# Kernel tuning notes

Hardware: AMD Instinct MI355X
Metric: run time of the kernel (lower is better)

## Reference

```python
import jax, jax.numpy as jnp
import numpy as np

EMBED_DIM = 1024
NUM_HEADS = 16
HEAD_DIM = EMBED_DIM // NUM_HEADS


def setup_inputs() -> dict:
    key = jax.random.key(0)
    ks = jax.random.split(key, 7)
    B, S, D = 2, 2048, EMBED_DIM
    scale = 1.0 / np.sqrt(D)
    return {
        "query": jax.random.normal(ks[0], (B, S, D), dtype=jnp.float32),
        "key": jax.random.normal(ks[1], (B, S, D), dtype=jnp.float32),
        "value": jax.random.normal(ks[2], (B, S, D), dtype=jnp.float32),
        "W_qkv": jax.random.normal(ks[3], (D, 3 * D), dtype=jnp.float32) * scale,
        "b_qkv": jnp.zeros((3 * D,), dtype=jnp.float32),
        "W_out": jax.random.normal(ks[4], (D, D), dtype=jnp.float32) * scale,
        "b_out": jnp.zeros((D,), dtype=jnp.float32),
    }


def reference(query, key, value, W_qkv, b_qkv, W_out, b_out):
    # NOTE: the original torch forward ignores `key` and `value` — q,k,v all
    # come from qkv_proj(query). We keep them as args for signature fidelity.
    B, S, D = query.shape
    H, hd = NUM_HEADS, HEAD_DIM
    scale = hd ** -0.5

    qkv = query @ W_qkv + b_qkv                      # [B, S, 3D]
    qkv = qkv.reshape(B, S, 3, H, hd)
    q = jnp.transpose(qkv[:, :, 0], (0, 2, 1, 3))    # [B, H, S, hd]
    k = jnp.transpose(qkv[:, :, 1], (0, 2, 1, 3))
    v = jnp.transpose(qkv[:, :, 2], (0, 2, 1, 3))

    scores = jnp.einsum("bhsd,bhtd->bhst", q, k) * scale  # [B, H, S, S]
    attn = jax.nn.softmax(scores, axis=-1)
    out = jnp.einsum("bhst,bhtd->bhsd", attn, v)           # [B, H, S, hd]
    out = jnp.transpose(out, (0, 2, 1, 3)).reshape(B, S, D)
    return out @ W_out + b_out
```

## Files before the change

### kernel.cpp

```cpp
#include <hip/hip_runtime.h>
#include <stdint.h>

#define DEV static __device__ __forceinline__

typedef __attribute__((ext_vector_type(4))) float f32x4;
typedef __attribute__((ext_vector_type(8))) short bf16x8;
typedef bf16x8 __attribute__((may_alias)) bf16x8_a;
typedef __attribute__((ext_vector_type(2))) unsigned int u32x2;
typedef u32x2 __attribute__((may_alias)) u32x2_a;

DEV unsigned short f2bf(float f) {
  union { float f; unsigned int u; } v; v.f = f;
  return (unsigned short)((v.u + 0x7FFFu + ((v.u >> 16) & 1u)) >> 16);
}

DEV float bf2f(unsigned short s) {
  union { unsigned int u; float f; } v; v.u = ((unsigned int)s) << 16;
  return v.f;
}

DEV float fast_exp2(float x) {
  float r;
  asm("v_exp_f32 %0, %1" : "=v"(r) : "v"(x));
  return r;
}

DEV unsigned int pktrunc(float lo, float hi) {
  union { float f; unsigned int u; } a, b; a.f = lo; b.f = hi;
  return __builtin_amdgcn_perm(b.u, a.u, 0x07060302u);
}

DEV void gload_lds16(const void* g, void* l) {
  __builtin_amdgcn_global_load_lds(
      (const __attribute__((address_space(1))) unsigned int*)g,
      (__attribute__((address_space(3))) unsigned int*)l, 16, 0, 0);
}

__global__ void cast_bf16_k(const float4* __restrict__ in, ushort4* __restrict__ out, int n4) {
  int i = blockIdx.x * 256 + threadIdx.x;
  if (i >= n4) return;
  float4 f = in[i];
  ushort4 o; o.x = f2bf(f.x); o.y = f2bf(f.y); o.z = f2bf(f.z); o.w = f2bf(f.w);
  out[i] = o;
}

__global__ __launch_bounds__(256) void transpose_bf16_k(const float* __restrict__ in,
                                                        unsigned short* __restrict__ out,
                                                        int R, int C) {
  __shared__ float tile[32][33];
  const int t = threadIdx.x;
  const int r = t >> 3, c4 = (t & 7) << 2;
  const int tr = blockIdx.y << 5, tc = blockIdx.x << 5;
  const float4 v = *(const float4*)(in + (size_t)(tr + r) * C + tc + c4);
  tile[r][c4] = v.x; tile[r][c4 + 1] = v.y; tile[r][c4 + 2] = v.z; tile[r][c4 + 3] = v.w;
  __syncthreads();
  ushort4 o;
  o.x = f2bf(tile[c4][r]); o.y = f2bf(tile[c4 + 1][r]);
  o.z = f2bf(tile[c4 + 2][r]); o.w = f2bf(tile[c4 + 3][r]);
  *(ushort4*)(out + (size_t)(tc + r) * R + tr + c4) = o;
}

template <int EPI, int BN>
__global__ __launch_bounds__(256) void gemm_bt(const unsigned short* __restrict__ A,
                                               const unsigned short* __restrict__ BT,
                                               const float* __restrict__ bias,
                                               float* __restrict__ Cout,
                                               unsigned short* __restrict__ q_buf,
                                               unsigned short* __restrict__ k_buf,
                                               unsigned short* __restrict__ vT_buf,
                                               int M, int N, int K) {
  constexpr int MI = (BN == 128) ? 4 : 2;
  constexpr int MW = MI * 16;
  __shared__ unsigned short As[2][128 * 32];
  __shared__ unsigned short Bs[2][BN * 32];
  const int t = threadIdx.x, w = t >> 6, l = t & 63;
  const int wm = (BN == 128) ? (w >> 1) : w;
  const int wn = (BN == 128) ? (w & 1) : 0;
  const int lg = l >> 4, ln = l & 15;

  const int xcd = blockIdx.x & 7, jb = blockIdx.x >> 3;
  const int m0 = (xcd * 4 + (jb & 3)) * 128;
  const int n0 = (jb >> 2) * BN;

  const int srow = w * 16 + (l >> 2);
  const int schunk = (l & 3) ^ ((l >> 3) & 3);
  const int dchunk = l & 3;

  f32x4 acc[MI][4] = {};

#define STAGE_G(buf, k0)                                                                              \
  do {                                                                                                \
    gload_lds16(A + (size_t)(m0 + srow) * K + (k0) + schunk * 8, &As[buf][srow * 32 + dchunk * 8]);   \
    gload_lds16(A + (size_t)(m0 + srow + 64) * K + (k0) + schunk * 8,                                 \
                &As[buf][(srow + 64) * 32 + dchunk * 8]);                                             \
    gload_lds16(BT + (size_t)(n0 + srow) * K + (k0) + schunk * 8, &Bs[buf][srow * 32 + dchunk * 8]);  \
    if (BN == 128)                                                                                    \
      gload_lds16(BT + (size_t)(n0 + srow + 64) * K + (k0) + schunk * 8,                              \
                  &Bs[buf][(srow + 64) * 32 + dchunk * 8]);                                           \
  } while (0)

  STAGE_G(0, 0);
  __syncthreads();

  const int rsw = (ln >> 1) & 3;
  const int rchunk = (lg ^ rsw) << 3;
  const int nit = K >> 5;
  for (int it = 0; it < nit; ++it) {
    const int buf = it & 1;
    if (it + 1 < nit) STAGE_G(buf ^ 1, (it + 1) * 32);

    bf16x8 af[MI], bfr[4];
#pragma unroll
    for (int mi = 0; mi < MI; ++mi)
      af[mi] = *(const bf16x8_a*)&As[buf][(wm * MW + mi * 16 + ln) * 32 + rchunk];
#pragma unroll
    for (int ni = 0; ni < 4; ++ni)
      bfr[ni] = *(const bf16x8_a*)&Bs[buf][(wn * 64 + ni * 16 + ln) * 32 + rchunk];
#pragma unroll
    for (int mi = 0; mi < MI; ++mi)
#pragma unroll
      for (int ni = 0; ni < 4; ++ni)
        acc[mi][ni] = __builtin_amdgcn_mfma_f32_16x16x32_bf16(af[mi], bfr[ni], acc[mi][ni], 0, 0, 0);

    __syncthreads();
  }
#undef STAGE_G

#pragma unroll
  for (int ni = 0; ni < 4; ++ni) {
    const int c = n0 + wn * 64 + ni * 16 + ln;
    const float bv = bias[c];
    if (EPI == 1) {
      const int which = c >> 10;
      const int h = (c >> 6) & 15;
      const int d = c & 63;
#pragma unroll
      for (int mi = 0; mi < MI; ++mi) {
        const int mrow = m0 + wm * MW + mi * 16 + lg * 4;
        const int b = mrow >> 11, s = mrow & 2047;
        const size_t bh = (size_t)(b * 16 + h);
        f32x4 v = acc[mi][ni];
        if (which == 0) {
          const float QSCALE = 0.125f * 1.44269504088896340736f;
          unsigned short* dst = q_buf + (bh * 2048 + s) * 64 + d;
#pragma unroll
          for (int r = 0; r < 4; ++r) dst[(size_t)r * 64] = f2bf((v[r] + bv) * QSCALE);
        } else if (which == 1) {
          unsigned short* dst = k_buf + (bh * 2048 + s) * 64 + d;
#pragma unroll
          for (int r = 0; r < 4; ++r) dst[(size_t)r * 64] = f2bf(v[r] + bv);
        } else {
          unsigned short* dst = vT_buf + (bh * 64 + d) * 2048 + s;
          ushort4 o4;
          o4.x = f2bf(v[0] + bv); o4.y = f2bf(v[1] + bv); o4.z = f2bf(v[2] + bv); o4.w = f2bf(v[3] + bv);
          *(ushort4*)dst = o4;
        }
      }
    } else {
#pragma unroll
      for (int mi = 0; mi < MI; ++mi) {
        const int mrow = m0 + wm * MW + mi * 16 + lg * 4;
        f32x4 v = acc[mi][ni];
#pragma unroll
        for (int r = 0; r < 4; ++r) Cout[(size_t)(mrow + r) * N + c] = v[r] + bv;
      }
    }
  }
}

template <int SPLIT>
__global__ __launch_bounds__(256, 3) void attn_k(const unsigned short* __restrict__ Qb,
                                                 const unsigned short* __restrict__ Kb,
                                                 const unsigned short* __restrict__ Vt,
                                                 unsigned short* __restrict__ AO,
                                                 unsigned short* __restrict__ Opart,
                                                 float* __restrict__ lpart) {
  constexpr int NT = 32 / SPLIT;
  const float SHIFT = -15.9943754f;
  const float CINV  = 0.99610895f;
  __shared__ unsigned short Ks[2][64 * 64];
  __shared__ unsigned short Vs[2][64 * 64];
  __shared__ unsigned short Ps[4][32 * 64];

  const int t = threadIdx.x, w = t >> 6, l = t & 63;
  const int lg = l >> 4, ln = l & 15;
  const int xcd = blockIdx.x & 7, idx = blockIdx.x >> 3;
  const int bh = xcd * 4 + (idx & 3);
  const int qt = (SPLIT == 2) ? ((idx >> 2) & 15) : (idx >> 2);
  const int half = (SPLIT == 2) ? (idx >> 6) : 0;
  const int b = bh >> 4, h = bh & 15;
  const unsigned short* Q = Qb + (size_t)bh * 2048 * 64;
  const unsigned short* K = Kb + (size_t)bh * 2048 * 64 + (size_t)half * NT * 64 * 64;
  const unsigned short* V = Vt + (size_t)bh * 64 * 2048 + half * NT * 64;
  const int qbase = qt * 128 + w * 32;

  const int srow = t >> 3;
  const int scol = ((t & 7) ^ (srow & 7)) << 3;
  const int dcol = (t & 7) << 3;

  bf16x8 qf[2][2];
#pragma unroll
  for (int nj = 0; nj < 2; ++nj)
#pragma unroll
    for (int kd = 0; kd < 2; ++kd)
      qf[nj][kd] = *(const bf16x8_a*)(Q + (size_t)(qbase + nj * 16 + ln) * 64 + kd * 32 + lg * 8);

  f32x4 o[2][4] = {};
  float l0r = 0.f, l1r = 0.f;

  {
    gload_lds16(K + (size_t)srow * 64 + scol,        &Ks[0][srow * 64 + dcol]);
    gload_lds16(K + (size_t)(srow + 32) * 64 + scol, &Ks[0][(srow + 32) * 64 + dcol]);
    gload_lds16(V + (size_t)srow * 2048 + scol,        &Vs[0][srow * 64 + dcol]);
    gload_lds16(V + (size_t)(srow + 32) * 2048 + scol, &Vs[0][(srow + 32) * 64 + dcol]);
  }
  __syncthreads();

  for (int tk = 0; tk < NT; ++tk) {
    const int cur = tk & 1;
    if (tk < NT - 1) {
      const int k1 = (tk + 1) * 64;
      const unsigned short* Kg = K + (size_t)k1 * 64;
      const unsigned short* Vg = V + k1;
      gload_lds16(Kg + (size_t)srow * 64 + scol,        &Ks[cur ^ 1][srow * 64 + dcol]);
      gload_lds16(Kg + (size_t)(srow + 32) * 64 + scol, &Ks[cur ^ 1][(srow + 32) * 64 + dcol]);
      gload_lds16(Vg + (size_t)srow * 2048 + scol,        &Vs[cur ^ 1][srow * 64 + dcol]);
      gload_lds16(Vg + (size_t)(srow + 32) * 2048 + scol, &Vs[cur ^ 1][(srow + 32) * 64 + dcol]);
    }

    bf16x8 kf[4][2];
#pragma unroll
    for (int mk = 0; mk < 4; ++mk)
#pragma unroll
      for (int kd = 0; kd < 2; ++kd)
        kf[mk][kd] = *(const bf16x8_a*)&Ks[cur][(mk * 16 + ln) * 64 + (((kd * 4 + lg) ^ (ln & 7)) << 3)];

    f32x4 sa[4][2] = {};
#pragma unroll
    for (int mk = 0; mk < 4; ++mk)
#pragma unroll
      for (int nj = 0; nj < 2; ++nj)
#pragma unroll
        for (int kd = 0; kd < 2; ++kd)
          sa[mk][nj] = __builtin_amdgcn_mfma_f32_16x16x32_bf16(kf[mk][kd], qf[nj][kd], sa[mk][nj], 0, 0, 0);

    bf16x8 vf[4][2];
#pragma unroll
    for (int nd = 0; nd < 4; ++nd)
#pragma unroll
      for (int ks = 0; ks < 2; ++ks)
        vf[nd][ks] = *(const bf16x8_a*)&Vs[cur][(nd * 16 + ln) * 64 + (((ks * 4 + lg) ^ (ln & 7)) << 3)];

    float rs0 = 0.f, rs1 = 0.f;
#pragma unroll
    for (int mk = 0; mk < 4; ++mk)
#pragma unroll
      for (int nj = 0; nj < 2; ++nj) {
        const float p0 = fast_exp2(sa[mk][nj][0] + SHIFT);
        const float p1 = fast_exp2(sa[mk][nj][1] + SHIFT);
        const float p2 = fast_exp2(sa[mk][nj][2] + SHIFT);
        const float p3 = fast_exp2(sa[mk][nj][3] + SHIFT);
        if (nj) rs1 += (p0 + p1) + (p2 + p3); else rs0 += (p0 + p1) + (p2 + p3);
        u32x2 pk;
        pk.x = pktrunc(p0, p1);
        pk.y = pktrunc(p2, p3);
        const int wcol = ((mk * 32 + lg * 8) ^ ((ln & 7) << 4)) >> 1;
        *(u32x2_a*)&Ps[w][(nj * 16 + ln) * 64 + wcol] = pk;
      }
    rs0 += __shfl_xor(rs0, 16); rs0 += __shfl_xor(rs0, 32);
    rs1 += __shfl_xor(rs1, 16); rs1 += __shfl_xor(rs1, 32);
    l0r += rs0;
    l1r += rs1;

#pragma unroll
    for (int ks = 0; ks < 2; ++ks) {
      const int rcol = ((ks * 64 + lg * 16) ^ ((ln & 7) << 4)) >> 1;
      const bf16x8 pf0 = *(const bf16x8_a*)&Ps[w][ln * 64 + rcol];
      const bf16x8 pf1 = *(const bf16x8_a*)&Ps[w][(16 + ln) * 64 + rcol];
#pragma unroll
      for (int nd = 0; nd < 4; ++nd) {
        o[0][nd] = __builtin_amdgcn_mfma_f32_16x16x32_bf16(pf0, vf[nd][ks], o[0][nd], 0, 0, 0);
        o[1][nd] = __builtin_amdgcn_mfma_f32_16x16x32_bf16(pf1, vf[nd][ks], o[1][nd], 0, 0, 0);
      }
    }

    __syncthreads();
  }

  l0r *= CINV;
  l1r *= CINV;

  if (SPLIT == 2) {
    const size_t pbase = ((size_t)(half * 32 + bh) * 2048 + qbase);
#pragma unroll
    for (int mi = 0; mi < 2; ++mi)
#pragma unroll
      for (int nd = 0; nd < 4; ++nd)
#pragma unroll
        for (int r = 0; r < 4; ++r)
          Opart[(pbase + mi * 16 + lg * 4 + r) * 64 + nd * 16 + ln] = f2bf(o[mi][nd][r]);
    if (lg == 0) {
      lpart[pbase + ln] = l0r;
      lpart[pbase + 16 + ln] = l1r;
    }
  } else {
    const float i0v = 1.0f / l0r, i1v = 1.0f / l1r;
    float i0[4], i1[4];
#pragma unroll
    for (int r = 0; r < 4; ++r) {
      const int src = lg * 4 + r;
      i0[r] = __shfl(i0v, src);
      i1[r] = __shfl(i1v, src);
    }
#pragma unroll
    for (int mi = 0; mi < 2; ++mi)
#pragma unroll
      for (int nd = 0; nd < 4; ++nd)
#pragma unroll
        for (int r = 0; r < 4; ++r) {
          const float iv = mi ? i1[r] : i0[r];
          const size_t row = (size_t)b * 2048 + qbase + mi * 16 + lg * 4 + r;
          AO[row * 1024 + h * 64 + nd * 16 + ln] = f2bf(o[mi][nd][r] * iv);
        }
  }
}

__global__ __launch_bounds__(256) void merge_k(const unsigned short* __restrict__ Opart,
                                               const float* __restrict__ lpart,
                                               unsigned short* __restrict__ AO) {
  const int u = blockIdx.x * 256 + threadIdx.x;
  const int c8 = u & 7, s = (u >> 3) & 2047, bh = u >> 14;
  const int b = bh >> 4, h = bh & 15;
  const size_t r0 = (size_t)bh * 2048 + s;
  const size_t r1 = (size_t)(32 + bh) * 2048 + s;
  const bf16x8 a0 = *(const bf16x8_a*)(Opart + r0 * 64 + c8 * 8);
  const bf16x8 a1 = *(const bf16x8_a*)(Opart + r1 * 64 + c8 * 8);
  const float inv = 1.0f / (lpart[r0] + lpart[r1]);
  bf16x8 oo;
#pragma unroll
  for (int i = 0; i < 8; ++i)
    oo[i] = (short)f2bf((bf2f((unsigned short)a0[i]) + bf2f((unsigned short)a1[i])) * inv);
  *(bf16x8_a*)(AO + ((size_t)b * 2048 + s) * 1024 + h * 64 + c8 * 8) = oo;
}

extern "C" void kernel_launch(void* const* d_in, const int* in_sizes, int n_in,
                              void* d_out, int out_size, void* d_ws, size_t ws_size,
                              hipStream_t stream) {
  const float* query = (const float*)d_in[0];
  const float* W_qkv = (const float*)d_in[3];
  const float* b_qkv = (const float*)d_in[4];
  const float* W_out = (const float*)d_in[5];
  const float* b_out = (const float*)d_in[6];
  float* out = (float*)d_out;
  char* ws = (char*)d_ws;

  unsigned short* Xb    = (unsigned short*)(ws);
  unsigned short* WqkvT = (unsigned short*)(ws + 8388608);
  unsigned short* WoutT = (unsigned short*)(ws + 14680064);
  unsigned short* qb    = (unsigned short*)(ws + 16777216);
  unsigned short* kb    = (unsigned short*)(ws + 25165824);
  unsigned short* vT    = (unsigned short*)(ws + 33554432);
  unsigned short* Opart = (unsigned short*)(ws + 41943040);
  float*          lpart = (float*)(ws + 58720256);
  const bool split2 = ws_size >= 59244544;
  unsigned short* AO    = Xb;

  cast_bf16_k<<<4096, 256, 0, stream>>>((const float4*)query, (ushort4*)Xb, 1048576);
  transpose_bf16_k<<<dim3(96, 32), 256, 0, stream>>>(W_qkv, WqkvT, 1024, 3072);
  transpose_bf16_k<<<dim3(32, 32), 256, 0, stream>>>(W_out, WoutT, 1024, 1024);
  gemm_bt<1, 128><<<768, 256, 0, stream>>>(Xb, WqkvT, b_qkv, nullptr, qb, kb, vT, 4096, 3072, 1024);
  if (split2) {
    attn_k<2><<<1024, 256, 0, stream>>>(qb, kb, vT, nullptr, Opart, lpart);
    merge_k<<<2048, 256, 0, stream>>>(Opart, lpart, AO);
  } else {
    attn_k<1><<<512, 256, 0, stream>>>(qb, kb, vT, AO, nullptr, nullptr);
  }
  gemm_bt<0, 64><<<512, 256, 0, stream>>>(AO, WoutT, b_out, out, nullptr, nullptr, nullptr, 4096, 1024, 1024);
}
```

Measured before the change: 123.7 us.

## Switch attention to 32x32x16 MFMA and keep P in registers

Result: no change. 123.0 us (-0.5%).

```diff
diff --git a/kernel.cpp b/kernel.cpp
--- a/kernel.cpp
+++ b/kernel.cpp
@@ -4,6 +4,7 @@
 #define DEV static __device__ __forceinline__
 
 typedef __attribute__((ext_vector_type(4))) float f32x4;
+typedef __attribute__((ext_vector_type(16))) float f32x16;
 typedef __attribute__((ext_vector_type(8))) short bf16x8;
 typedef bf16x8 __attribute__((may_alias)) bf16x8_a;
 typedef __attribute__((ext_vector_type(2))) unsigned int u32x2;
@@ -150,7 +151,8 @@
 #pragma unroll
           for (int r = 0; r < 4; ++r) dst[(size_t)r * 64] = f2bf(v[r] + bv);
         } else {
-          unsigned short* dst = vT_buf + (bh * 64 + d) * 2048 + s;
+          const int sp = (s & ~12) | ((s & 4) << 1) | ((s & 8) >> 1);
+          unsigned short* dst = vT_buf + (bh * 64 + d) * 2048 + sp;
           ushort4 o4;
           o4.x = f2bf(v[0] + bv); o4.y = f2bf(v[1] + bv); o4.z = f2bf(v[2] + bv); o4.w = f2bf(v[3] + bv);
           *(ushort4*)dst = o4;
@@ -169,7 +171,7 @@
 }
 
 template <int SPLIT>
-__global__ __launch_bounds__(256, 3) void attn_k(const unsigned short* __restrict__ Qb,
+__global__ __launch_bounds__(256, 4) void attn_k(const unsigned short* __restrict__ Qb,
                                                  const unsigned short* __restrict__ Kb,
                                                  const unsigned short* __restrict__ Vt,
                                                  unsigned short* __restrict__ AO,
@@ -180,10 +182,9 @@
   const float CINV  = 0.99610895f;
   __shared__ unsigned short Ks[2][64 * 64];
   __shared__ unsigned short Vs[2][64 * 64];
-  __shared__ unsigned short Ps[4][32 * 64];
 
   const int t = threadIdx.x, w = t >> 6, l = t & 63;
-  const int lg = l >> 4, ln = l & 15;
+  const int l31 = l & 31, lh = l >> 5;
   const int xcd = blockIdx.x & 7, idx = blockIdx.x >> 3;
   const int bh = xcd * 4 + (idx & 3);
   const int qt = (SPLIT == 2) ? ((idx >> 2) & 15) : (idx >> 2);
@@ -198,15 +199,13 @@
   const int scol = ((t & 7) ^ (srow & 7)) << 3;
   const int dcol = (t & 7) << 3;
 
-  bf16x8 qf[2][2];
-#pragma unroll
-  for (int nj = 0; nj < 2; ++nj)
-#pragma unroll
-    for (int kd = 0; kd < 2; ++kd)
-      qf[nj][kd] = *(const bf16x8_a*)(Q + (size_t)(qbase + nj * 16 + ln) * 64 + kd * 32 + lg * 8);
-
-  f32x4 o[2][4] = {};
-  float l0r = 0.f, l1r = 0.f;
+  bf16x8 qf[4];
+#pragma unroll
+  for (int kd = 0; kd < 4; ++kd)
+    qf[kd] = *(const bf16x8_a*)(Q + (size_t)(qbase + l31) * 64 + kd * 16 + lh * 8);
+
+  f32x16 o32[2] = {};
+  float lr = 0.f;
 
   {
     gload_lds16(K + (size_t)srow * 64 + scol,        &Ks[0][srow * 64 + dcol]);
@@ -228,100 +227,83 @@
       gload_lds16(Vg + (size_t)(srow + 32) * 2048 + scol, &Vs[cur ^ 1][(srow + 32) * 64 + dcol]);
     }
 
-    bf16x8 kf[4][2];
-#pragma unroll
-    for (int mk = 0; mk < 4; ++mk)
-#pragma unroll
-      for (int kd = 0; kd < 2; ++kd)
-        kf[mk][kd] = *(const bf16x8_a*)&Ks[cur][(mk * 16 + ln) * 64 + (((kd * 4 + lg) ^ (ln & 7)) << 3)];
-
-    f32x4 sa[4][2] = {};
-#pragma unroll
-    for (int mk = 0; mk < 4; ++mk)
-#pragma unroll
-      for (int nj = 0; nj < 2; ++nj)
-#pragma unroll
-        for (int kd = 0; kd < 2; ++kd)
-          sa[mk][nj] = __builtin_amdgcn_mfma_f32_16x16x32_bf16(kf[mk][kd], qf[nj][kd], sa[mk][nj], 0, 0, 0);
-
-    bf16x8 vf[4][2];
-#pragma unroll
-    for (int nd = 0; nd < 4; ++nd)
-#pragma unroll
-      for (int ks = 0; ks < 2; ++ks)
-        vf[nd][ks] = *(const bf16x8_a*)&Vs[cur][(nd * 16 + ln) * 64 + (((ks * 4 + lg) ^ (ln & 7)) << 3)];
-
-    float rs0 = 0.f, rs1 = 0.f;
-#pragma unroll
-    for (int mk = 0; mk < 4; ++mk)
-#pragma unroll
-      for (int nj = 0; nj < 2; ++nj) {
-        const float p0 = fast_exp2(sa[mk][nj][0] + SHIFT);
-        const float p1 = fast_exp2(sa[mk][nj][1] + SHIFT);
-        const float p2 = fast_exp2(sa[mk][nj][2] + SHIFT);
-        const float p3 = fast_exp2(sa[mk][nj][3] + SHIFT);
-        if (nj) rs1 += (p0 + p1) + (p2 + p3); else rs0 += (p0 + p1) + (p2 + p3);
-        u32x2 pk;
-        pk.x = pktrunc(p0, p1);
-        pk.y = pktrunc(p2, p3);
-        const int wcol = ((mk * 32 + lg * 8) ^ ((ln & 7) << 4)) >> 1;
-        *(u32x2_a*)&Ps[w][(nj * 16 + ln) * 64 + wcol] = pk;
-      }
-    rs0 += __shfl_xor(rs0, 16); rs0 += __shfl_xor(rs0, 32);
-    rs1 += __shfl_xor(rs1, 16); rs1 += __shfl_xor(rs1, 32);
-    l0r += rs0;
-    l1r += rs1;
-
-#pragma unroll
-    for (int ks = 0; ks < 2; ++ks) {
-      const int rcol = ((ks * 64 + lg * 16) ^ ((ln & 7) << 4)) >> 1;
-      const bf16x8 pf0 = *(const bf16x8_a*)&Ps[w][ln * 64 + rcol];
-      const bf16x8 pf1 = *(const bf16x8_a*)&Ps[w][(16 + ln) * 64 + rcol];
-#pragma unroll
-      for (int nd = 0; nd < 4; ++nd) {
-        o[0][nd] = __builtin_amdgcn_mfma_f32_16x16x32_bf16(pf0, vf[nd][ks], o[0][nd], 0, 0, 0);
-        o[1][nd] = __builtin_amdgcn_mfma_f32_16x16x32_bf16(pf1, vf[nd][ks], o[1][nd], 0, 0, 0);
-      }
+    f32x16 sa[2] = {};
+#pragma unroll
+    for (int m2 = 0; m2 < 2; ++m2)
+#pragma unroll
+      for (int kd = 0; kd < 4; ++kd) {
+        const bf16x8 kf = *(const bf16x8_a*)
+            &Ks[cur][(m2 * 32 + l31) * 64 + (((kd * 2 + lh) ^ (l & 7)) << 3)];
+        sa[m2] = __builtin_amdgcn_mfma_f32_32x32x16_bf16(kf, qf[kd], sa[m2], 0, 0, 0);
+      }
+
+    bf16x8 vf0[4];
+#pragma unroll
+    for (int ksI = 0; ksI < 4; ++ksI)
+      vf0[ksI] = *(const bf16x8_a*)&Vs[cur][l31 * 64 + (((ksI * 2 + lh) ^ (l & 7)) << 3)];
+
+    unsigned int pk[2][8];
+    float rs = 0.f;
+#pragma unroll
+    for (int m2 = 0; m2 < 2; ++m2) {
+      float p[16];
+#pragma unroll
+      for (int r = 0; r < 16; ++r) {
+        p[r] = fast_exp2(sa[m2][r] + SHIFT);
+        rs += p[r];
+      }
+#pragma unroll
+      for (int u = 0; u < 8; ++u)
+        pk[m2][u] = pktrunc(p[2 * u], p[2 * u + 1]);
     }
+    rs += __shfl_xor(rs, 32);
+    lr += rs;
+
+#pragma unroll
+    for (int m2 = 0; m2 < 2; ++m2)
+#pragma unroll
+      for (int ks2 = 0; ks2 < 2; ++ks2) {
+        const int ksI = m2 * 2 + ks2;
+        union { unsigned int u[4]; bf16x8 v; } pa;
+        pa.u[0] = pk[m2][ks2 * 4 + 0];
+        pa.u[1] = pk[m2][ks2 * 4 + 1];
+        pa.u[2] = pk[m2][ks2 * 4 + 2];
+        pa.u[3] = pk[m2][ks2 * 4 + 3];
+        const bf16x8 vf1 = *(const bf16x8_a*)
+            &Vs[cur][(32 + l31) * 64 + (((ksI * 2 + lh) ^ (l & 7)) << 3)];
+        o32[0] = __builtin_amdgcn_mfma_f32_32x32x16_bf16(pa.v, vf0[ksI], o32[0], 0, 0, 0);
+        o32[1] = __builtin_amdgcn_mfma_f32_32x32x16_bf16(pa.v, vf1, o32[1], 0, 0, 0);
+      }
 
     __syncthreads();
   }
 
-  l0r *= CINV;
-  l1r *= CINV;
+  lr *= CINV;
 
   if (SPLIT == 2) {
     const size_t pbase = ((size_t)(half * 32 + bh) * 2048 + qbase);
 #pragma unroll
-    for (int mi = 0; mi < 2; ++mi)
-#pragma unroll
-      for (int nd = 0; nd < 4; ++nd)
-#pragma unroll
-        for (int r = 0; r < 4; ++r)
-          Opart[(pbase + mi * 16 + lg * 4 + r) * 64 + nd * 16 + ln] = f2bf(o[mi][nd][r]);
-    if (lg == 0) {
-      lpart[pbase + ln] = l0r;
-      lpart[pbase + 16 + ln] = l1r;
-    }
+    for (int nb = 0; nb < 2; ++nb)
+#pragma unroll
+      for (int r = 0; r < 16; ++r) {
+        const int qrow = (r & 3) + 8 * (r >> 2) + 4 * lh;
+        Opart[(pbase + qrow) * 64 + nb * 32 + l31] = f2bf(o32[nb][r]);
+      }
+    if (l < 32) lpart[pbase + l] = lr;
   } else {
-    const float i0v = 1.0f / l0r, i1v = 1.0f / l1r;
-    float i0[4], i1[4];
-#pragma unroll
-    for (int r = 0; r < 4; ++r) {
-      const int src = lg * 4 + r;
-      i0[r] = __shfl(i0v, src);
-      i1[r] = __shfl(i1v, src);
-    }
-#pragma unroll
-    for (int mi = 0; mi < 2; ++mi)
-#pragma unroll
-      for (int nd = 0; nd < 4; ++nd)
-#pragma unroll
-        for (int r = 0; r < 4; ++r) {
-          const float iv = mi ? i1[r] : i0[r];
-          const size_t row = (size_t)b * 2048 + qbase + mi * 16 + lg * 4 + r;
-          AO[row * 1024 + h * 64 + nd * 16 + ln] = f2bf(o[mi][nd][r] * iv);
-        }
+    const float inv = 1.0f / lr;
+    float iv[16];
+#pragma unroll
+    for (int r = 0; r < 16; ++r)
+      iv[r] = __shfl(inv, (r & 3) + 8 * (r >> 2) + 4 * lh);
+#pragma unroll
+    for (int nb = 0; nb < 2; ++nb)
+#pragma unroll
+      for (int r = 0; r < 16; ++r) {
+        const int qrow = (r & 3) + 8 * (r >> 2) + 4 * lh;
+        const size_t row = (size_t)b * 2048 + qbase + qrow;
+        AO[row * 1024 + h * 64 + nb * 32 + l31] = f2bf(o32[nb][r] * iv[r]);
+      }
   }
 }
 
```
